# Kernel optimization log

Hardware: AMD Instinct MI355X
Metric: run time of the kernel (lower is better)

The kernel has to match this reference:

```python
import jax, jax.numpy as jnp
import numpy as np

# S=enc seq len (<= 2**ADD), B=batch, E=embed, H=hidden=controller, ADD=address bits,
# HA/HC = number of mode-1/mode-2 pointers, T=decode steps, OUT=out_size
S, B, E, H, ADD, HA, HC, T, OUT = 256, 128, 512, 512, 8, 2, 1, 64, 512
G = 3 * H  # GRU gate dim


def gru_cell(x, h, Wih, Whh, bih, bhh):
    gi = x @ Wih.T + bih
    gh = h @ Whh.T + bhh
    ir, iz, inn = jnp.split(gi, 3, -1)
    hr, hz, hn = jnp.split(gh, 3, -1)
    r = jax.nn.sigmoid(ir + hr)
    z = jax.nn.sigmoid(iz + hz)
    n = jnp.tanh(inn + r * hn)
    return (1.0 - z) * n + z * h


def run_gru(xs, h0, Wih, Whh, bih, bhh):
    def step(h, x):
        h2 = gru_cell(x, h, Wih, Whh, bih, bhh)
        return h2, h2
    return jax.lax.scan(step, h0, xs)


def setup_inputs():
    key = jax.random.key(0)
    ki = iter(jax.random.split(key, 48))
    def rn(shape, s=0.05):
        return jax.random.normal(next(ki), shape, jnp.float32) * s
    inp = {}
    inp['src'] = jax.random.normal(next(ki), (S, B, E), jnp.float32)
    inp['tgt'] = jax.random.normal(next(ki), (T, B, E), jnp.float32)
    # external address memory: 8-bit binary codes, rolled by a random start per batch
    rng = np.random.default_rng(0)
    base = ((np.arange(2 ** ADD)[:, None] & (1 << np.arange(ADD))[None, :]) != 0).astype(np.float32)
    starts = rng.integers(0, 2 ** ADD, size=B)
    A = np.stack([np.roll(base, int(s), axis=0)[:S] for s in starts], axis=1)  # (S,B,ADD)
    inp['A'] = jnp.asarray(A)
    # encoder bidirectional GRU
    inp['enc_Wih_f'] = rn((G, E)); inp['enc_Whh_f'] = rn((G, H))
    inp['enc_bih_f'] = rn((G,)); inp['enc_bhh_f'] = rn((G,))
    inp['enc_Wih_b'] = rn((G, E)); inp['enc_Whh_b'] = rn((G, H))
    inp['enc_bih_b'] = rn((G,)); inp['enc_bhh_b'] = rn((G,))
    # decoder Bahdanau attention
    inp['dec_attn_W'] = rn((H, 2 * H)); inp['dec_attn_b'] = rn((H,)); inp['dec_attn_v'] = rn((H,))
    # decoder GRU: input = [embedded(E + HA*H), context(H)]
    DIN = E + HA * H + H
    inp['dec_Wih'] = rn((G, DIN)); inp['dec_Whh'] = rn((G, H))
    inp['dec_bih'] = rn((G,)); inp['dec_bhh'] = rn((G,))
    inp['dec_out_W'] = rn((H, 2 * H)); inp['dec_out_b'] = rn((H,))
    # pointer units (stacked over HA)
    inp['pu_Wih'] = rn((HA, G, ADD)); inp['pu_Whh'] = rn((HA, G, H))
    inp['pu_bih'] = rn((HA, G)); inp['pu_bhh'] = rn((HA, G))
    inp['pu_qW'] = rn((HA, H, H)); inp['pu_qb'] = rn((HA, H))
    inp['pu_AmapW'] = rn((HA, ADD, ADD)); inp['pu_Amapb'] = rn((HA, ADD))
    inp['pu_qproj'] = rn((HA, H, H)); inp['pu_kproj'] = rn((HA, H, ADD)); inp['pu_vproj'] = rn((HA, H, H))
    inp['pu_inb'] = rn((HA, 3 * H))
    inp['pu_oproj'] = rn((HA, H, H)); inp['pu_ob'] = rn((HA, H))
    # content-based attention (add_att, 1 head)
    inp['aa_qproj'] = rn((H, H)); inp['aa_kproj'] = rn((H, H)); inp['aa_vproj'] = rn((H, H))
    inp['aa_inb'] = rn((3 * H,))
    inp['aa_oproj'] = rn((H, H)); inp['aa_ob'] = rn((H,))
    # tohs (HC=1) and output head
    inp['toh_W'] = rn((H, HA * H)); inp['toh_b'] = rn((H,))
    inp['out_W'] = rn((OUT, H * (HA + 1 + HC))); inp['out_b'] = rn((OUT,))
    inp['target_length'] = T
    return inp


def _forward(src, tgt, A,
             enc_Wih_f, enc_Whh_f, enc_bih_f, enc_bhh_f,
             enc_Wih_b, enc_Whh_b, enc_bih_b, enc_bhh_b,
             dec_attn_W, dec_attn_b, dec_attn_v,
             dec_Wih, dec_Whh, dec_bih, dec_bhh, dec_out_W, dec_out_b,
             pu_Wih, pu_Whh, pu_bih, pu_bhh, pu_qW, pu_qb, pu_AmapW, pu_Amapb,
             pu_qproj, pu_kproj, pu_vproj, pu_inb, pu_oproj, pu_ob,
             aa_qproj, aa_kproj, aa_vproj, aa_inb, aa_oproj, aa_ob,
             toh_W, toh_b, out_W, out_b):
    h0 = jnp.zeros((B, H), src.dtype)
    hTf, ysf = run_gru(src, h0, enc_Wih_f, enc_Whh_f, enc_bih_f, enc_bhh_f)
    hTb, ysb = run_gru(src[::-1], h0, enc_Wih_b, enc_Whh_b, enc_bih_b, enc_bhh_b)
    enc = ysf + ysb[::-1]                      # (S,B,H) sum of directions
    enc_bsh = jnp.swapaxes(enc, 0, 1)          # (B,S,H)
    A_bsa = A.reshape(B, S, ADD)               # faithful to torch .view(A.shape[1], A.shape[0], -1)
    scale = 1.0 / jnp.sqrt(jnp.asarray(H, src.dtype))
    # hoisted step-invariant K/V projections for the HA pointer units
    pu_bq, pu_bk, pu_bv = jnp.split(pu_inb, 3, axis=-1)                       # (HA,H) each
    Am = jnp.einsum('sba,uca->usbc', A, pu_AmapW) + pu_Amapb[:, None, None, :]
    Kp = jnp.einsum('usba,uha->usbh', Am, pu_kproj) + pu_bk[:, None, None, :]  # (HA,S,B,H)
    Vp = jnp.einsum('sbe,uhe->usbh', enc, pu_vproj) + pu_bv[:, None, None, :]  # (HA,S,B,H)
    aa_bq, aa_bk, aa_bv = jnp.split(aa_inb, 3)
    Kc = enc @ aa_kproj.T + aa_bk              # (S,B,H)
    Vc = enc @ aa_vproj.T + aa_bv

    def punit(ptr, hid, Wih, Whh, bih, bhh, qW, qb, qproj, bq, Kpu, Vpu, oproj, ob):
        hid2 = gru_cell(ptr, hid, Wih, Whh, bih, bhh)              # (B,H)
        q = (hid2 @ qW.T + qb) @ qproj.T + bq                       # (B,H)
        aw = jax.nn.softmax(jnp.einsum('bh,sbh->bs', q, Kpu) * scale, -1)
        cur_val = jnp.einsum('bs,sbh->bh', aw, Vpu) @ oproj.T + ob  # (B,H)
        cur_add = jnp.einsum('bs,bsa->ba', aw, A_bsa)               # (B,ADD)
        return cur_val, cur_add, hid2

    punit_v = jax.vmap(punit)

    ptrs0 = jnp.stack([A[0] if i % 2 == 0 else A[S - 1] for i in range(HA)])  # (HA,B,ADD)
    hida0 = jnp.zeros((HA, B, H), src.dtype)
    carry0 = (tgt[0], hTf, hida0, ptrs0)

    def step(carry, trg_t):
        out_emb, dec_h, hida, ptrs = carry
        cv1, cadd, hida2 = punit_v(ptrs, hida, pu_Wih, pu_Whh, pu_bih, pu_bhh,
                                   pu_qW, pu_qb, pu_qproj, pu_bq, Kp, Vp, pu_oproj, pu_ob)
        cv1_cat = jnp.swapaxes(cv1, 0, 1).reshape(B, HA * H)
        # Bahdanau attention of decoder hidden over encoder outputs
        cat = jnp.concatenate([jnp.broadcast_to(dec_h[:, None, :], (B, S, H)), enc_bsh], -1)
        energy = jax.nn.relu(cat @ dec_attn_W.T + dec_attn_b)       # (B,S,H)
        aw = jax.nn.softmax(energy @ dec_attn_v, -1)                # (B,S)
        ctx = jnp.einsum('bs,bsh->bh', aw, enc_bsh)
        rnn_in = jnp.concatenate([out_emb, cv1_cat, ctx], -1)       # [embedded, context]
        dec_h2 = gru_cell(rnn_in, dec_h, dec_Wih, dec_Whh, dec_bih, dec_bhh)
        dec_out = jnp.concatenate([dec_h2, ctx], -1) @ dec_out_W.T + dec_out_b  # (B,H)
        # content-based pointer (HC=1)
        qc = (cv1_cat @ toh_W.T + toh_b) @ aa_qproj.T + aa_bq
        awc = jax.nn.softmax(jnp.einsum('bh,sbh->bs', qc, Kc) * scale, -1)
        cv2 = jnp.einsum('bs,sbh->bh', awc, Vc) @ aa_oproj.T + aa_ob
        out_t = jnp.concatenate([dec_out, cv1_cat, cv2], -1) @ out_W.T + out_b
        return (trg_t, dec_h2, hida2, cadd), out_t

    _, outs = jax.lax.scan(step, carry0, tgt)
    return outs  # (T,B,OUT)


def reference(src, tgt, A,
              enc_Wih_f, enc_Whh_f, enc_bih_f, enc_bhh_f,
              enc_Wih_b, enc_Whh_b, enc_bih_b, enc_bhh_b,
              dec_attn_W, dec_attn_b, dec_attn_v,
              dec_Wih, dec_Whh, dec_bih, dec_bhh, dec_out_W, dec_out_b,
              pu_Wih, pu_Whh, pu_bih, pu_bhh, pu_qW, pu_qb, pu_AmapW, pu_Amapb,
              pu_qproj, pu_kproj, pu_vproj, pu_inb, pu_oproj, pu_ob,
              aa_qproj, aa_kproj, aa_vproj, aa_inb, aa_oproj, aa_ob,
              toh_W, toh_b, out_W, out_b, target_length):
    return _forward(src, tgt, A,
                    enc_Wih_f, enc_Whh_f, enc_bih_f, enc_bhh_f,
                    enc_Wih_b, enc_Whh_b, enc_bih_b, enc_bhh_b,
                    dec_attn_W, dec_attn_b, dec_attn_v,
                    dec_Wih, dec_Whh, dec_bih, dec_bhh, dec_out_W, dec_out_b,
                    pu_Wih, pu_Whh, pu_bih, pu_bhh, pu_qW, pu_qb, pu_AmapW, pu_Amapb,
                    pu_qproj, pu_kproj, pu_vproj, pu_inb, pu_oproj, pu_ob,
                    aa_qproj, aa_kproj, aa_vproj, aa_inb, aa_oproj, aa_ob,
                    toh_W, toh_b, out_W, out_b)
```

## Files before the change

kernel.cpp:

```cpp
#include <hip/hip_runtime.h>

typedef unsigned short u16;
typedef unsigned int u32;

#define DEVI __device__ __forceinline__

constexpr float SCALE_ATT = 0.04419417382415922f;

constexpr size_t OFF_GI    = 0;
constexpr size_t OFF_ENC   = OFF_GI    + 4ull*2*32*128*1536;
constexpr size_t OFF_EATT  = OFF_ENC   + 2ull*256*128*512;
constexpr size_t OFF_AM    = OFF_EATT  + 2ull*256*128*512;
constexpr size_t OFF_HF    = OFF_AM    + 4ull*2*256*128*8;
constexpr size_t OFF_HB    = OFF_HF    + 4ull*2*128*512;
constexpr size_t OFF_HFB   = OFF_HB    + 4ull*2*128*512;
constexpr size_t OFF_HBB   = OFF_HFB   + 2ull*2*128*512;
constexpr size_t OFF_HIDA  = OFF_HBB   + 2ull*2*128*512;
constexpr size_t OFF_HIDAB = OFF_HIDA  + 4ull*2*2*128*512;
constexpr size_t OFF_BAR   = OFF_HIDAB + 2ull*2*2*128*512;
constexpr size_t OFF_ZEND  = OFF_BAR   + 49152;
constexpr size_t OFF_DECH  = OFF_ZEND;
constexpr size_t OFF_DECHB = OFF_DECH  + 4ull*2*128*512;
constexpr size_t OFF_PTRS  = OFF_DECHB + 2ull*2*128*512;
constexpr size_t OFF_VPRE  = OFF_PTRS  + 4ull*2*128*8;
// ... 467 lines not shown
  const float* ap = Ain + ((size_t)b * 256 + t) * 8;
  float av[8];
  {
    float4 v0 = *(const float4*)ap;
    float4 v1 = *(const float4*)(ap + 4);
    av[0]=v0.x; av[1]=v0.y; av[2]=v0.z; av[3]=v0.w;
    av[4]=v1.x; av[5]=v1.y; av[6]=v1.z; av[7]=v1.w;
  }

  float inv[2];
  for (int u = 0; u < 2; u++){
    float s_ = su[u];
    float* sc = u ? sc1 : sc0;
    float m = s_;
    #pragma unroll
    for (int off = 32; off > 0; off >>= 1) m = fmaxf(m, __shfl_xor(m, off));
    if (lane == 0) red[w] = m;
    __syncthreads();
    float mx = fmaxf(fmaxf(red[0], red[1]), fmaxf(red[2], red[3]));
    float e = __expf(s_ - mx); sc[t] = e;
    float ca[9];
    ca[8] = e;
    #pragma unroll
    for (int a2 = 0; a2 < 8; a2++) ca[a2] = e * av[a2];
    #pragma unroll
    for (int j = 0; j < 9; j++){
      #pragma unroll
      for (int off = 32; off > 0; off >>= 1) ca[j] += __shfl_xor(ca[j], off);
    }
    if (lane == 0){
      #pragma unroll
      for (int j = 0; j < 9; j++) wred[w * 9 + j] = ca[j];
    }
    __syncthreads();
    if (t < 9){
      float v = wred[t] + wred[9 + t] + wred[18 + t] + wred[27 + t];
      if (t < 8) cd[u * 8 + t] = v;
      else red[4 + u] = v;
    }
    __syncthreads();
    inv[u] = 1.f / red[4 + u];
  }
  if (t < 8){
    st4_sys(&ptrs[((size_t)0 * 128 + b) * 8 + t], cd[t] * inv[0]);
    st4_sys(&ptrs[((size_t)128 + b) * 8 + t],     cd[8 + t] * inv[1]);
  }

  float a00 = 0.f, a01 = 0.f, a10 = 0.f, a11 = 0.f;
  const u16* ep = enc + (size_t)b * 512;
  #pragma unroll 16
  for (int s2 = 0; s2 < 256; s2++){
    float w0 = sc0[s2], w1 = sc1[s2];
    u32 pv = *(const u32*)(ep + (size_t)s2 * 65536 + 2 * t);
    float v0 = b2f((u16)pv);
    float v1 = b2f((u16)(pv >> 16));
    a00 += w0 * v0; a01 += w0 * v1; a10 += w1 * v0; a11 += w1 * v1;
  }
  float* vp = vpre + (size_t)b * 1024;
  st4_sys(&vp[2 * t], a00 * inv[0]);           st4_sys(&vp[2 * t + 1], a01 * inv[0]);
  st4_sys(&vp[512 + 2 * t], a10 * inv[1]);     st4_sys(&vp[512 + 2 * t + 1], a11 * inv[1]);
}

DEVI void dev_bahd(int b, const u16* eatt, const float* dpart, const float* vvec,
                   const u16* enc, float* ctx, float* fs)
{
  int t = threadIdx.x, lane = t & 63, w = t >> 6;
  float* dp = fs; float* vv = fs + 512; float* sc = fs + 1024; float* red = fs + 1280;
  dp[t] = ld4f_sys(dpart + (size_t)b * 512 + t);
  dp[t + 256] = ld4f_sys(dpart + (size_t)b * 512 + t + 256);
  vv[t] = vvec[t]; vv[t + 256] = vvec[t + 256];
  __syncthreads();
  float4 d0 = *(float4*)&dp[lane * 8], d1 = *(float4*)&dp[lane * 8 + 4];
  float4 v0 = *(float4*)&vv[lane * 8], v1 = *(float4*)&vv[lane * 8 + 4];
  for (int sb = 0; sb < 256; sb += 32){
    uint4 vl[8];
    #pragma unroll
    for (int i = 0; i < 8; i++){
      int s = sb + i * 4 + w;
      vl[i] = *(const uint4*)(eatt + ((size_t)s * 128 + b) * 512 + lane * 8);
    }
    #pragma unroll
    for (int i = 0; i < 8; i++){
      const u16* h = (const u16*)&vl[i];
      float r = fmaxf(0.f, b2f(h[0]) + d0.x) * v0.x + fmaxf(0.f, b2f(h[1]) + d0.y) * v0.y
              + fmaxf(0.f, b2f(h[2]) + d0.z) * v0.z + fmaxf(0.f, b2f(h[3]) + d0.w) * v0.w
              + fmaxf(0.f, b2f(h[4]) + d1.x) * v1.x + fmaxf(0.f, b2f(h[5]) + d1.y) * v1.y
              + fmaxf(0.f, b2f(h[6]) + d1.z) * v1.z + fmaxf(0.f, b2f(h[7]) + d1.w) * v1.w;
      #pragma unroll
      for (int off = 32; off > 0; off >>= 1) r += __shfl_xor(r, off);
      if (lane == 0) sc[sb + i * 4 + w] = r;
    }
  }
  __syncthreads();
  float s0 = sc[t];
  float m = s0;
  #pragma unroll
  for (int off = 32; off > 0; off >>= 1) m = fmaxf(m, __shfl_xor(m, off));
  if (lane == 0) red[w] = m;
  __syncthreads();
  float mx = fmaxf(fmaxf(red[0], red[1]), fmaxf(red[2], red[3]));
  float e = __expf(s0 - mx); sc[t] = e;
  float sum = e;
  #pragma unroll
  for (int off = 32; off > 0; off >>= 1) sum += __shfl_xor(sum, off);
  if (lane == 0) red[4 + w] = sum;
  __syncthreads();
  float inv = 1.f / (red[4] + red[5] + red[6] + red[7]);
  float a0 = 0.f, a1 = 0.f;
  const u16* ep = enc + (size_t)b * 512;
  #pragma unroll 16
  for (int s2 = 0; s2 < 256; s2++){
    float wgt = sc[s2];
    u32 pv = *(const u32*)(ep + (size_t)s2 * 65536 + 2 * t);
    a0 += wgt * b2f((u16)pv);
    a1 += wgt * b2f((u16)(pv >> 16));
  }
  st4_sys(&ctx[(size_t)b * 512 + 2 * t], a0 * inv);
  st4_sys(&ctx[(size_t)b * 512 + 2 * t + 1], a1 * inv);
}

DEVI void dev_cattn(int b, const float* qck, const u16* enc, float* cv2p, float* fs)
{
  int t = threadIdx.x, lane = t & 63, w = t >> 6;
  float* qv = fs; float* sc = fs + 1024; float* red = fs + 1280;
  qv[t] = ld4f_sys(qck + (size_t)b * 520 + t);
  qv[t + 256] = ld4f_sys(qck + (size_t)b * 520 + t + 256);
  __syncthreads();
  float qc0 = ld4f_sys(qck + (size_t)b * 520 + 512);
  float4 q0 = *(float4*)&qv[lane * 8], q1 = *(float4*)&qv[lane * 8 + 4];
  for (int sb = 0; sb < 256; sb += 32){
    uint4 vl[8];
    #pragma unroll
    for (int i = 0; i < 8; i++){
      int s = sb + i * 4 + w;
      vl[i] = *(const uint4*)(enc + ((size_t)s * 128 + b) * 512 + lane * 8);
    }
    #pragma unroll
    for (int i = 0; i < 8; i++){
      const u16* h = (const u16*)&vl[i];
      float r = b2f(h[0])*q0.x + b2f(h[1])*q0.y + b2f(h[2])*q0.z + b2f(h[3])*q0.w
              + b2f(h[4])*q1.x + b2f(h[5])*q1.y + b2f(h[6])*q1.z + b2f(h[7])*q1.w;
      #pragma unroll
      for (int off = 32; off > 0; off >>= 1) r += __shfl_xor(r, off);
      if (lane == 0) sc[sb + i * 4 + w] = (r + qc0) * SCALE_ATT;
    }
  }
  __syncthreads();
  float s0 = sc[t];
  float m = s0;
  #pragma unroll
  for (int off = 32; off > 0; off >>= 1) m = fmaxf(m, __shfl_xor(m, off));
  if (lane == 0) red[w] = m;
  __syncthreads();
  float mx = fmaxf(fmaxf(red[0], red[1]), fmaxf(red[2], red[3]));
  float e = __expf(s0 - mx); sc[t] = e;
  float sum = e;
  #pragma unroll
  for (int off = 32; off > 0; off >>= 1) sum += __shfl_xor(sum, off);
  if (lane == 0) red[4 + w] = sum;
  __syncthreads();
  float inv = 1.f / (red[4] + red[5] + red[6] + red[7]);
  float a0 = 0.f, a1 = 0.f;
  const u16* ep = enc + (size_t)b * 512;
  #pragma unroll 16
  for (int s2 = 0; s2 < 256; s2++){
    float wgt = sc[s2];
    u32 pv = *(const u32*)(ep + (size_t)s2 * 65536 + 2 * t);
    a0 += wgt * b2f((u16)pv);
    a1 += wgt * b2f((u16)(pv >> 16));
  }
  st4_sys(&cv2p[(size_t)b * 512 + 2 * t], a0 * inv);
  st4_sys(&cv2p[(size_t)b * 512 + 2 * t + 1], a1 * inv);
}

DEVI void dev_outcvt(int b, const float* outt, const float* outb2, float* dst)
{
  int t = threadIdx.x;
  #pragma unroll
  for (int rep = 0; rep < 2; rep++){
    int o = t + rep * 256;
    float s = ld4f_sys(outt + (size_t)b * 512 + o) + ld4f_sys(outt + 65536 + (size_t)b * 512 + o)
            + ld4f_sys(outt + 131072 + (size_t)b * 512 + o) + ld4f_sys(outt + 196608 + (size_t)b * 512 + o);
    dst[(size_t)b * 512 + o] = s + outb2[o];
  }
}

struct EncArgs {
  const float *WhhF, *WhhB, *giF, *giB;
  const float *bihF, *bhhF, *bihB, *bhhB;
  float *HF, *HB; u16 *HFB, *HBB, *ENC;
  u32 *BAR; int bar0;
  int s0;
};

__global__ __launch_bounds__(256) void k_enc(EncArgs a)
{
  __shared__ short Bw[24576];
  __shared__ short Al[4096];
  int blk = blockIdx.x;
  int d = blk >> 5, gt = blk & 31;
  int t = threadIdx.x, lane = t & 63, w = t >> 6;

  const float* Whh = d ? a.WhhB : a.WhhF;
  for (int c = t; c < 3072; c += 256){
    int brow = c >> 6, kc = c & 63;
    int grow = (brow >> 4) * 512 + gt * 16 + (brow & 15);
    const float* wp = Whh + (size_t)grow * 512 + kc * 8;
    *(uint4*)&Bw[((kc * 48) + brow) * 8] = cvt8(*(const float4*)wp, *(const float4*)(wp + 4));
  }
  const float* bih = d ? a.bihB : a.bihF;
  const float* bhh = d ? a.bhhB : a.bhhF;
  int gcol = gt * 16 + (lane & 15);
  float bir = bih[gcol],        bhr = bhh[gcol];
  float biz = bih[512 + gcol],  bhz = bhh[512 + gcol];
  float bin = bih[1024 + gcol], bhn = bhh[1024 + gcol];
  float* hf_base = d ? a.HB : a.HF;
  u16*   hb_base = d ? a.HBB : a.HFB;
  const float* gi_base = d ? a.giB : a.giF;
  __syncthreads();

  for (int si = 0; si < 32; si++){
    int s = a.s0 + si;
    const u16* hb = hb_base + (size_t)(s & 1) * 65536;
    const float* hf = hf_base + (size_t)(s & 1) * 65536;
    float* hnf = hf_base + (size_t)((s + 1) & 1) * 65536;
    u16* hnb = hb_base + (size_t)((s + 1) & 1) * 65536;
    u16* eacc = a.ENC + (size_t)(d ? 255 - s : s) * 65536;

    ffrag zz4 = {0.f, 0.f, 0.f, 0.f};
    ffrag acc[2][3];
    #pragma unroll
    for (int i = 0; i < 2; i++)
      #pragma unroll
      for (int j = 0; j < 3; j++) acc[i][j] = zz4;

    for (int ki = 0; ki < 16; ki++){
      int k0 = ki * 32;
      int row0 = t >> 2, kq0 = t & 3;
      int row1 = (t + 256) >> 2, kq1 = (t + 256) & 3;
      vu4 hv0, hv1;
      ld16_nw(hb + (size_t)row0 * 512 + k0 + kq0 * 8, hv0);
      ld16_nw(hb + (size_t)row1 * 512 + k0 + kq1 * 8, hv1);
      vm_drain();
      *(vu4*)&Al[(((row0 >> 4) << 6) + (kq0 << 4) + (row0 & 15)) * 8] = hv0;
      *(vu4*)&Al[(((row1 >> 4) << 6) + (kq1 << 4) + (row1 & 15)) * 8] = hv1;
      __syncthreads();
      bfrag af[2], bv[3];
      #pragma unroll
      for (int fr = 0; fr < 2; fr++) af[fr] = *(bfrag*)&Al[(((w * 2 + fr) * 64) + lane) * 8];
      #pragma unroll
      for (int fc = 0; fc < 3; fc++) bv[fc] = *(bfrag*)&Bw[(((ki * 4 + (lane >> 4)) * 48) + fc * 16 + (lane & 15)) * 8];
      #pragma unroll
      for (int fr = 0; fr < 2; fr++)
        #pragma unroll
        for (int fc = 0; fc < 3; fc++)
          acc[fr][fc] = __builtin_amdgcn_mfma_f32_16x16x32_bf16(af[fr], bv[fc], acc[fr][fc], 0, 0, 0);
      __syncthreads();
    }

    const float* gp0 = gi_base + (size_t)si * 196608;
    #pragma unroll
    for (int fr = 0; fr < 2; fr++){
      #pragma unroll
      for (int i = 0; i < 4; i++){
        int brow = w * 32 + fr * 16 + ((lane >> 4) << 2) + i;
        const float* gp = gp0 + (size_t)brow * 1536;
        float gr_ = gp[gcol], gz_ = gp[512 + gcol], gn_ = gp[1024 + gcol];
        float hold = ld4f_sys(hf + (size_t)brow * 512 + gcol);
        float r  = sigmf_(gr_ + acc[fr][0][i] + bir + bhr);
        float zg = sigmf_(gz_ + acc[fr][1][i] + biz + bhz);
        float n  = tanhf_(gn_ + bin + r * (acc[fr][2][i] + bhn));
        float hn = (1.f - zg) * n + zg * hold;
        size_t idx = (size_t)brow * 512 + gcol;
        st4_sys(hnf + idx, hn);
        st2_sys(hnb + idx, f2b(hn));
        eacc[idx] = f2b(b2f(eacc[idx]) + hn);
      }
    }
    gridbar2(a.BAR + BAR_ENCF, a.BAR + BAR_ENCGO, (u32)(a.s0 + si + 1), 64, blk, 0);
  }
}

struct DecArgs {
  const float *tgt, *Ag, *AM, *KA, *CAE, *dattW, *dattv;
  const float *puWhh, *puWih, *pubih, *pubhh;
  const float *dWhh, *DBIH2, *dbhh, *VKE2, *OUTB2;
  const u16 *ENC, *EATT, *DWF, *MKTW, *OWF;
  float *HIDA; u16 *HIDAB;
  float *DECH; u16 *DECHB;
  float *HF0; u16 *HFB0;
  float *PTRS, *VPRE, *CTX, *DPART, *QCK, *CV2P, *GIDEC, *OUTT, *out;
  u32 *BAR;
};

__global__ __launch_bounds__(256) void k_dec(DecArgs a)
{
  __shared__ short Al[4096];
  __shared__ short Bl[4096];
  __shared__ float fs[1600];
  const int blk = blockIdx.x;
  const Seg4 S4SENT = {nullptr, 0, 0, 1 << 30, 0};
  u32* dF = a.BAR + BAR_DECF;
  u32* dG = a.BAR + BAR_DECGO;
  const int GATHER = 200;

  for (int st = 0; st < 64; st++){
    const float* hida_c  = a.HIDA  + (size_t)(st & 1) * 131072;
    float*       hida_n  = a.HIDA  + (size_t)((st + 1) & 1) * 131072;
    const u16*   hidab_c = a.HIDAB + (size_t)(st & 1) * 131072;
    u16*         hidab_n = a.HIDAB + (size_t)((st + 1) & 1) * 131072;
    const float* dech_c  = (st == 0) ? a.HF0  : a.DECH  + (size_t)((st + 1) & 1) * 65536;
    const u16*   dechb_c = (st == 0) ? a.HFB0 : a.DECHB + (size_t)((st + 1) & 1) * 65536;
    float*       dech_n  = a.DECH  + (size_t)(st & 1) * 65536;
    u16*         dechb_n = a.DECHB + (size_t)(st & 1) * 65536;
    u32 seq0 = (u32)(st * 5);

    if (blk < 32){
      int u = blk >> 4, g0 = (blk & 15) * 32;
      dev_gru3<1>(g0, hidab_c + (size_t)u * 65536, hida_c + (size_t)u * 65536,
                  a.puWhh + (size_t)u * 786432, nullptr,
                  a.PTRS + u * 1024, a.puWih + (size_t)u * 12288,
                  a.pubih + u * 1536, a.pubhh + u * 1536,
                  hida_n + (size_t)u * 65536, hidab_n + (size_t)u * 65536, Al, Bl);
    } else if (blk < 40){
      Z4 z;
      z.sg[0] = {dechb_c, 512, 0, 512, 1}; z.sg[1] = S4SENT; z.sg[2] = S4SENT; z.sg[3] = S4SENT;
      z.Bp = a.dattW; z.ldb = 1024; z.bf32 = 1; z.bias = nullptr;
      z.Cp = a.DPART; z.ldc = 512; z.cslab = 0; z.N = 512; z.K = 512;
      dev_mfma4<64>(z, blk - 32, 0, 1, Al, Bl);
    } else if (blk < 168 && st > 0){
      dev_outcvt(blk - 40, a.OUTT, a.OUTB2, a.out + (size_t)(st - 1) * 65536);
    }
    gridbar2(dF, dG, seq0 + 1, 256, blk, GATHER);

    if (blk < 128){
      dev_puattn(blk, hida_n, a.KA, a.CAE, a.AM, a.Ag, a.ENC, a.VPRE, a.PTRS, fs);
    } else {
      dev_bahd(blk - 128, a.EATT, a.DPART, a.dattv, a.ENC, a.CTX, fs);
    }
    gridbar2(dF, dG, seq0 + 2, 256, blk, GATHER);

    if (blk < 48){
      Z4 z;
      z.sg[0] = {a.tgt + (size_t)(st ? st - 1 : 0) * 65536, 512, 1, 512, 0};
      z.sg[1] = {a.VPRE, 1024, 1, 1024, 1};
      z.sg[2] = {a.CTX, 512, 1, 512, 1};
      z.sg[3] = S4SENT;
      z.Bp = a.DWF; z.ldb = 2048; z.bf32 = 0; z.bias = nullptr;
      z.Cp = a.GIDEC; z.ldc = 1536; z.cslab = 196608; z.N = 1536; z.K = 2048;
      dev_mfma4<128>(z, blk % 12, blk / 12, 4, Al, Bl);
    } else if (blk < 57){
      Z4 z;
      z.sg[0] = {a.VPRE, 1024, 1, 1024, 1}; z.sg[1] = S4SENT; z.sg[2] = S4SENT; z.sg[3] = S4SENT;
      z.Bp = a.MKTW; z.ldb = 1024; z.bf32 = 0; z.bias = a.VKE2;
      z.Cp = a.QCK; z.ldc = 520; z.cslab = 0; z.N = 513; z.K = 1024;
      dev_mfma4<64>(z, blk - 48, 0, 1, Al, Bl);
    }
    gridbar2(dF, dG, seq0 + 3, 256, blk, GATHER);

    if (blk < 16){
      dev_gru3<2>(blk * 32, dechb_c, dech_c, a.dWhh, a.GIDEC, nullptr, nullptr,
                  a.DBIH2, a.dbhh, dech_n, dechb_n, Al, Bl);
    } else if (blk < 144){
      dev_cattn(blk - 16, a.QCK, a.ENC, a.CV2P, fs);
    }
    gridbar2(dF, dG, seq0 + 4, 256, blk, GATHER);

    if (blk < 32){
      Z4 z;
      z.sg[0] = {dechb_n, 512, 0, 512, 1};
      z.sg[1] = {a.CTX, 512, 1, 512, 1};
      z.sg[2] = {a.VPRE, 1024, 1, 1024, 1};
      z.sg[3] = {a.CV2P, 512, 1, 512, 1};
      z.Bp = a.OWF; z.ldb = 2560; z.bf32 = 0; z.bias = nullptr;
      z.Cp = a.OUTT; z.ldc = 512; z.cslab = 65536; z.N = 512; z.K = 2560;
      dev_mfma4<64>(z, blk & 7, blk >> 3, 4, Al, Bl);
    }
    gridbar2(dF, dG, seq0 + 5, 256, blk, GATHER);
  }
  if (blk < 128) dev_outcvt(blk, a.OUTT, a.OUTB2, a.out + 63ull * 65536);
}

struct Job {
  const float* A; const float* B; const float* D; void* C;
  int Asm, Ask, Bsk, Bsn, Dsm, Dsn, Csm, Csn;
  int cbf, M, N, K, kind;
};
struct Jobs { Job j[24]; int nj; long long off[25]; };

__global__ __launch_bounds__(256) void k_setup(Jobs J)
{
  long long total = J.off[J.nj];
  for (long long tid = (long long)blockIdx.x * 256 + threadIdx.x; tid < total; tid += (long long)gridDim.x * 256){
    int ji = 0;
    while (tid >= J.off[ji + 1]) ji++;
    Job jb = J.j[ji];
    long long l = tid - J.off[ji];
    if (jb.kind == 0){
      int m = (int)(l / jb.N), n = (int)(l - (long long)m * jb.N);
      float acc = 0.f;
      const float* ap = jb.A + (size_t)m * jb.Asm;
      const float* bp = jb.B + (size_t)n * jb.Bsn;
      for (int k = 0; k < jb.K; k++)
        acc += ap[(size_t)k * jb.Ask] * bp[(size_t)k * jb.Bsk];
      if (jb.D) acc += jb.D[(size_t)m * jb.Dsm + (size_t)n * jb.Dsn];
      if (jb.cbf) ((u16*)jb.C)[(size_t)m * jb.Csm + (size_t)n * jb.Csn] = f2b(acc);
      else ((float*)jb.C)[(size_t)m * jb.Csm + (size_t)n * jb.Csn] = acc;
    } else if (jb.kind == 1){
      int m = (int)(l / jb.N), n = (int)(l - (long long)m * jb.N);
      ((u16*)jb.C)[(size_t)m * jb.Csm + (size_t)n * jb.Csn] = f2b(jb.A[(size_t)m * jb.Asm + (size_t)n * jb.Ask]);
    } else if (jb.kind == 2){
      int u = (int)(l >> 15), sb = (int)(l & 32767);
      float x[8];
      #pragma unroll
      for (int a2 = 0; a2 < 8; a2++) x[a2] = jb.A[(size_t)sb * 8 + a2];
      float* op = (float*)jb.C + ((size_t)u * 32768 + sb) * 8;
      #pragma unroll
      for (int c = 0; c < 8; c++){
        float acc = jb.D[u * 8 + c];
        #pragma unroll
        for (int a2 = 0; a2 < 8; a2++) acc += x[a2] * jb.B[(u * 8 + c) * 8 + a2];
        op[c] = acc;
      }
    } else {
      int u = (int)(l >> 10), r = (int)(l & 1023);
      int bb = r >> 3, aa = r & 7;
      int su = u ? 255 : 0;
      ((float*)jb.C)[l] = jb.A[((size_t)su * 128 + bb) * 8 + aa];
    }
  }
}

static inline Seg mkseg(const void* p, int ld, int f32, int K){ Seg s; s.p = p; s.ld = ld; s.f32 = f32; s.K = K; return s; }
static const Seg SENT = {nullptr, 0, 0, 1 << 30};

static inline void addJ(Jobs& JS, Job jb, long long cnt){
  JS.j[JS.nj] = jb;
  JS.off[JS.nj + 1] = JS.off[JS.nj] + cnt;
  JS.nj++;
}
static inline Job JG(const float* A, int Asm, int Ask, const float* B, int Bsk, int Bsn,
                     const float* D, int Dsm, int Dsn, void* C, int Csm, int Csn,
                     int cbf, int M, int N, int K, int kind = 0){
  Job j; j.A=A; j.B=B; j.D=D; j.C=C; j.Asm=Asm; j.Ask=Ask; j.Bsk=Bsk; j.Bsn=Bsn;
  j.Dsm=Dsm; j.Dsn=Dsn; j.Csm=Csm; j.Csn=Csn; j.cbf=cbf; j.M=M; j.N=N; j.K=K; j.kind=kind;
  return j;
}

extern "C" void kernel_launch(void* const* d_in, const int* in_sizes, int n_in,
                              void* d_out, int out_size, void* d_ws, size_t ws_size,
                              hipStream_t stream)
{
  (void)in_sizes; (void)out_size;
  if (n_in < 44 || ws_size < WS_NEED) return;

  const float* src   = (const float*)d_in[0];
  const float* tgt   = (const float*)d_in[1];
  const float* Ag    = (const float*)d_in[2];
  const float* eWihF = (const float*)d_in[3];
  const float* eWhhF = (const float*)d_in[4];
  const float* ebihF = (const float*)d_in[5];
  const float* ebhhF = (const float*)d_in[6];
  const float* eWihB = (const float*)d_in[7];
  const float* eWhhB = (const float*)d_in[8];
  const float* ebihB = (const float*)d_in[9];
  const float* ebhhB = (const float*)d_in[10];
  const float* dattW = (const float*)d_in[11];
  const float* dattb = (const float*)d_in[12];
  const float* dattv = (const float*)d_in[13];
  const float* dWih  = (const float*)d_in[14];
  const float* dWhh  = (const float*)d_in[15];
  const float* dbih  = (const float*)d_in[16];
  const float* dbhh  = (const float*)d_in[17];
  const float* doW   = (const float*)d_in[18];
  const float* dob   = (const float*)d_in[19];
  const float* puWih = (const float*)d_in[20];
  const float* puWhh = (const float*)d_in[21];
  const float* pubih = (const float*)d_in[22];
  const float* pubhh = (const float*)d_in[23];
  const float* puqW  = (const float*)d_in[24];
  const float* puqb  = (const float*)d_in[25];
  const float* puAW  = (const float*)d_in[26];
  const float* puAb  = (const float*)d_in[27];
  const float* puqp  = (const float*)d_in[28];
  const float* pukp  = (const float*)d_in[29];
  const float* puvp  = (const float*)d_in[30];
  const float* puinb = (const float*)d_in[31];
  const float* puop  = (const float*)d_in[32];
  const float* puob  = (const float*)d_in[33];
  const float* aaq   = (const float*)d_in[34];
  const float* aak   = (const float*)d_in[35];
  const float* aav   = (const float*)d_in[36];
  const float* aainb = (const float*)d_in[37];
  const float* aao   = (const float*)d_in[38];
  const float* aaob  = (const float*)d_in[39];
  const float* tohW  = (const float*)d_in[40];
  const float* tohb  = (const float*)d_in[41];
  const float* outW  = (const float*)d_in[42];
  const float* outb  = (const float*)d_in[43];

  char* ws = (char*)d_ws;
  float* GI    = (float*)(ws + OFF_GI);
  u16*   ENC   = (u16*)(ws + OFF_ENC);
  u16*   EATT  = (u16*)(ws + OFF_EATT);
  float* AM    = (float*)(ws + OFF_AM);
  float* HF    = (float*)(ws + OFF_HF);
  float* HB    = (float*)(ws + OFF_HB);
  u16*   HFB   = (u16*)(ws + OFF_HFB);
  u16*   HBB   = (u16*)(ws + OFF_HBB);
  float* HIDA  = (float*)(ws + OFF_HIDA);
  u16*   HIDAB = (u16*)(ws + OFF_HIDAB);
  u32*   BAR   = (u32*)(ws + OFF_BAR);
  float* DECH  = (float*)(ws + OFF_DECH);
  u16*   DECHB = (u16*)(ws + OFF_DECHB);
  float* PTRS  = (float*)(ws + OFF_PTRS);
  float* VPRE  = (float*)(ws + OFF_VPRE);
  float* CTX   = (float*)(ws + OFF_CTX);
  float* DPART = (float*)(ws + OFF_DPART);
  float* QCK   = (float*)(ws + OFF_QCK);
  float* CV2P  = (float*)(ws + OFF_CV2P);
  float* GIDEC = (float*)(ws + OFF_GIDEC);
  float* OUTT  = (float*)(ws + OFF_OUTT);
  float* WOVF  = (float*)(ws + OFF_WOVF);
  float* WOVCF = (float*)(ws + OFF_WOVCF);
  float* MKTF  = (float*)(ws + OFF_MKTF);
  u16*   DWF   = (u16*)(ws + OFF_DWF);
  u16*   MKTW  = (u16*)(ws + OFF_MKTW);
  u16*   OWF   = (u16*)(ws + OFF_OWF);
  float* BOV   = (float*)(ws + OFF_BOV);
  float* BOVC  = (float*)(ws + OFF_BOVC);
  float* KAx   = (float*)(ws + OFF_KA);
  float* CAE   = (float*)(ws + OFF_CAE);
  float* RT    = (float*)(ws + OFF_RT);
  float* BQC   = (float*)(ws + OFF_BQC);
  float* PMAT  = (float*)(ws + OFF_PMAT);
  float* CQ    = (float*)(ws + OFF_CQ);
  float* VKE2  = (float*)(ws + OFF_VKE2);
  float* DBIH2 = (float*)(ws + OFF_DBIH2);
  float* OUTB2 = (float*)(ws + OFF_OUTB2);

  hipMemsetAsync(ENC, 0, 2ull*256*128*512, stream);
  hipMemsetAsync(ws + OFF_HF, 0, OFF_ZEND - OFF_HF, stream);

  {
    Jobs S{}; S.nj = 0; S.off[0] = 0;
    for (int u = 0; u < 2; u++){
      const float* qp  = puqp + (size_t)u * 262144;
      const float* kp  = pukp + (size_t)u * 4096;
      float* RTu = RT + u * 8192;
      addJ(S, JG(qp, 1, 512, kp, 8, 1, nullptr, 0, 0, RTu, 16, 1, 0, 512, 8, 512), 4096);
      addJ(S, JG(qp, 1, 512, puinb + u*1536 + 512, 1, 0, nullptr, 0, 0, RTu + 8, 16, 1, 0, 512, 1, 512), 512);
      addJ(S, JG(qp, 512, 1, puqb + u*512, 1, 0, puinb + u*1536, 1, 0, BQC + u*512, 1, 1, 0, 512, 1, 512), 512);
      addJ(S, JG(puop + (size_t)u*262144, 512, 1, puvp + (size_t)u*262144, 512, 1, nullptr, 0, 0, WOVF + (size_t)u*262144, 512, 1, 0, 512, 512, 512), 262144);
      addJ(S, JG(puop + (size_t)u*262144, 512, 1, puinb + u*1536 + 1024, 1, 0, puob + u*512, 1, 0, BOV + u*512, 1, 1, 0, 512, 1, 512), 512);
    }
    addJ(S, JG(aao, 512, 1, aav, 512, 1, nullptr, 0, 0, WOVCF, 512, 1, 0, 512, 512, 512), 262144);
    addJ(S, JG(aao, 512, 1, aainb + 1024, 1, 0, aaob, 1, 0, BOVC, 1, 1, 0, 512, 1, 512), 512);
    addJ(S, JG(aaq, 1, 512, aak, 512, 1, nullptr, 0, 0, PMAT, 516, 1, 0, 512, 512, 512), 262144);
    addJ(S, JG(aaq, 1, 512, aainb + 512, 1, 0, nullptr, 0, 0, PMAT + 512, 516, 1, 0, 512, 1, 512), 512);
    addJ(S, JG(aaq, 512, 1, tohb, 1, 0, aainb, 1, 0, CQ, 1, 1, 0, 512, 1, 512), 512);
    addJ(S, JG(dWih, 2048, 1, nullptr, 0, 0, nullptr, 0, 0, DWF, 2048, 1, 1, 1536, 512, 0, 1), 786432);
    addJ(S, JG(dWih + 1536, 2048, 1, nullptr, 0, 0, nullptr, 0, 0, DWF + 1536, 2048, 1, 1, 1536, 512, 0, 1), 786432);
    addJ(S, JG(outW, 2048, 1, doW, 1024, 1, nullptr, 0, 0, OWF, 2560, 1, 1, 512, 1024, 512), 524288);
    addJ(S, JG(outW, 2048, 1, dob, 1, 0, outb, 1, 0, OUTB2, 1, 1, 0, 512, 1, 512), 512);
    addJ(S, JG(Ag, 0, 0, puAW, 0, 0, puAb, 0, 0, AM, 0, 0, 0, 0, 0, 0, 2), 65536);
    addJ(S, JG(Ag, 0, 0, nullptr, 0, 0, nullptr, 0, 0, PTRS, 0, 0, 0, 0, 0, 0, 3), 2048);
    k_setup<<<2048, 256, 0, stream>>>(S);
  }
  {
    Jobs S{}; S.nj = 0; S.off[0] = 0;
    for (int u = 0; u < 2; u++){
      const float* kp = pukp + (size_t)u * 4096;
      addJ(S, JG(puqW + (size_t)u*262144, 1, 512, RT + u*8192, 16, 1, nullptr, 0, 0, KAx + u*8192, 16, 1, 0, 512, 9, 512), 4608);
      addJ(S, JG(BQC + u*512, 0, 1, kp, 8, 1, nullptr, 0, 0, CAE + u*16, 0, 1, 0, 1, 8, 512), 8);
      addJ(S, JG(BQC + u*512, 0, 1, puinb + u*1536 + 512, 1, 0, nullptr, 0, 0, CAE + u*16 + 8, 0, 1, 0, 1, 1, 512), 1);
      addJ(S, JG(dWih + 512 + u*512, 2048, 1, WOVF + (size_t)u*262144, 512, 1, nullptr, 0, 0, DWF + 512 + u*512, 2048, 1, 1, 1536, 512, 512), 786432);
      addJ(S, JG(outW + 512 + u*512, 2048, 1, WOVF + (size_t)u*262144, 512, 1, nullptr, 0, 0, OWF + 1024 + u*512, 2560, 1, 1, 512, 512, 512), 262144);
    }
    addJ(S, JG(tohW, 1, 1024, PMAT, 516, 1, nullptr, 0, 0, MKTF, 1, 1024, 0, 1024, 513, 512), 525312);
    addJ(S, JG(CQ, 0, 1, aak, 512, 1, nullptr, 0, 0, VKE2, 0, 1, 0, 1, 512, 512), 512);
    addJ(S, JG(CQ, 0, 1, aainb + 512, 1, 0, nullptr, 0, 0, VKE2 + 512, 0, 1, 0, 1, 1, 512), 1);
    addJ(S, JG(dWih + 512, 2048, 1, BOV, 1, 0, dbih, 1, 0, DBIH2, 1, 1, 0, 1536, 1, 1024), 1536);
    addJ(S, JG(outW + 1536, 2048, 1, WOVCF, 512, 1, nullptr, 0, 0, OWF + 2048, 2560, 1, 1, 512, 512, 512), 262144);
    addJ(S, JG(outW + 512, 2048, 1, BOV, 1, 0, OUTB2, 1, 0, OUTB2, 1, 1, 0, 512, 1, 1536), 512);
    k_setup<<<2048, 256, 0, stream>>>(S);
  }
  {
    Jobs S{}; S.nj = 0; S.off[0] = 0;
    for (int u = 0; u < 2; u++)
      addJ(S, JG(MKTF + u*512, 1024, 1, WOVF + (size_t)u*262144, 512, 1, nullptr, 0, 0, MKTW + u*512, 1024, 1, 1, 513, 512, 512), 262656);
    addJ(S, JG(MKTF, 1024, 1, BOV, 1, 0, VKE2, 1, 0, VKE2, 1, 1, 0, 513, 1, 1024), 513);
    k_setup<<<1024, 256, 0, stream>>>(S);
  }

  for (int c = 0; c < 8; c++){
    int c0 = c * 32;
    NTA nt{};
    nt.tilesN = 12;
    for (int d = 0; d < 2; d++){
      NTZ& zz = nt.z[d];
      zz.sg[0] = mkseg(d == 0 ? (const void*)(src + (size_t)c0 * 65536) : (const void*)src, 512, 1, 512);
      zz.sg[1] = SENT; zz.sg[2] = SENT;
      zz.Bp = d ? eWihB : eWihF; zz.ldb = 512; zz.bf32 = 1;
      zz.bias = nullptr; zz.biasf32 = 0;
      zz.Cp = GI + (size_t)d * 6291456; zz.ldc = 1536; zz.cf32 = 1; zz.cslab = 0;
      zz.N = 1536; zz.rev_s0 = (d == 0) ? -1 : (255 - c0); zz.K = 512;
    }
    k_mfma_nt<128><<<dim3(32*12, 1, 2), 256, 0, stream>>>(nt);

    EncArgs ea;
    ea.WhhF = eWhhF; ea.WhhB = eWhhB;
    ea.giF = GI; ea.giB = GI + 6291456;
    ea.bihF = ebihF; ea.bhhF = ebhhF; ea.bihB = ebihB; ea.bhhB = ebhhB;
    ea.HF = HF; ea.HB = HB; ea.HFB = HFB; ea.HBB = HBB; ea.ENC = ENC;
    ea.BAR = BAR; ea.bar0 = c * 32;
    ea.s0 = c0;
    k_enc<<<dim3(64), dim3(256), 0, stream>>>(ea);
  }

  {
    NTA nt{};
    nt.tilesN = 4;
    NTZ& zz = nt.z[0];
    zz.sg[0] = mkseg(ENC, 512, 0, 512); zz.sg[1] = SENT; zz.sg[2] = SENT;
    zz.Bp = dattW + 512; zz.ldb = 1024; zz.bf32 = 1;
    zz.bias = dattb; zz.biasf32 = 1;
    zz.Cp = EATT; zz.ldc = 512; zz.cf32 = 0; zz.cslab = 0;
    zz.N = 512; zz.rev_s0 = -1; zz.K = 512;
    k_mfma_nt<128><<<dim3(256*4, 1, 1), 256, 0, stream>>>(nt);
  }

  {
    DecArgs da;
    da.tgt = tgt; da.Ag = Ag; da.AM = AM; da.KA = KAx; da.CAE = CAE;
    da.dattW = dattW; da.dattv = dattv;
    da.puWhh = puWhh; da.puWih = puWih; da.pubih = pubih; da.pubhh = pubhh;
    da.dWhh = dWhh; da.DBIH2 = DBIH2; da.dbhh = dbhh; da.VKE2 = VKE2; da.OUTB2 = OUTB2;
    da.ENC = ENC; da.EATT = EATT; da.DWF = DWF; da.MKTW = MKTW; da.OWF = OWF;
    da.HIDA = HIDA; da.HIDAB = HIDAB; da.DECH = DECH; da.DECHB = DECHB;
    da.HF0 = HF; da.HFB0 = HFB;
    da.PTRS = PTRS; da.VPRE = VPRE; da.CTX = CTX; da.DPART = DPART;
    da.QCK = QCK; da.CV2P = CV2P; da.GIDEC = GIDEC; da.OUTT = OUTT;
    da.out = (float*)d_out;
    da.BAR = BAR;
    k_dec<<<dim3(256), dim3(256), 0, stream>>>(da);
  }
}
```

Before: 22.81 ms.

## Software-pipeline decoder step to remove one grid barrier per step

Moves the pointer-unit GRU for step st+1 and the decoder attention-projection GEMM for the next step into earlier phases of the current step, run on otherwise idle blocks. The prologue computes step 0's versions before the loop. This cuts the grid barriers per decode step from five to four, and the output conversion moves to another phase. It also raises the barrier GATHER parameter. The risk is data hazards: the PU GRU for st+1 now runs right after puattn reads hida_n, and those reads must be complete before the buffers are overwritten.

```diff
diff --git a/kernel.cpp b/kernel.cpp
--- a/kernel.cpp
+++ b/kernel.cpp
@@ -793,43 +793,49 @@
   const Seg4 S4SENT = {nullptr, 0, 0, 1 << 30, 0};
   u32* dF = a.BAR + BAR_DECF;
   u32* dG = a.BAR + BAR_DECGO;
-  const int GATHER = 200;
+  const int GATHER = 230;
+
+  #define PU_GRU(s_, u_, g0_) do { \
+    int s__ = (s_); int u__ = (u_); \
+    const u16*  pc_ = a.HIDAB + (size_t)(s__ & 1) * 131072 + (size_t)u__ * 65536; \
+    const float* pf_ = a.HIDA  + (size_t)(s__ & 1) * 131072 + (size_t)u__ * 65536; \
+    float* pn_  = a.HIDA  + (size_t)((s__ + 1) & 1) * 131072 + (size_t)u__ * 65536; \
+    u16*   pnb_ = a.HIDAB + (size_t)((s__ + 1) & 1) * 131072 + (size_t)u__ * 65536; \
+    dev_gru3<1>((g0_), pc_, pf_, a.puWhh + (size_t)u__ * 786432, nullptr, \
+                a.PTRS + u__ * 1024, a.puWih + (size_t)u__ * 12288, \
+                a.pubih + u__ * 1536, a.pubhh + u__ * 1536, pn_, pnb_, Al, Bl); \
+  } while(0)
+
+  #define DPART_GEMM(srcb_, tn_) do { \
+    Z4 z_; \
+    z_.sg[0] = {(srcb_), 512, 0, 512, 1}; z_.sg[1] = S4SENT; z_.sg[2] = S4SENT; z_.sg[3] = S4SENT; \
+    z_.Bp = a.dattW; z_.ldb = 1024; z_.bf32 = 1; z_.bias = nullptr; \
+    z_.Cp = a.DPART; z_.ldc = 512; z_.cslab = 0; z_.N = 512; z_.K = 512; \
+    dev_mfma4<64>(z_, (tn_), 0, 1, Al, Bl); \
+  } while(0)
+
+  if (blk < 32){
+    int u = blk >> 4, g0 = (blk & 15) * 32;
+    PU_GRU(0, u, g0);
+  } else if (blk < 40){
+    DPART_GEMM(a.HFB0, blk - 32);
+  }
+  gridbar2(dF, dG, 1u, 256, blk, GATHER);
 
   for (int st = 0; st < 64; st++){
-    const float* hida_c  = a.HIDA  + (size_t)(st & 1) * 131072;
-    float*       hida_n  = a.HIDA  + (size_t)((st + 1) & 1) * 131072;
-    const u16*   hidab_c = a.HIDAB + (size_t)(st & 1) * 131072;
-    u16*         hidab_n = a.HIDAB + (size_t)((st + 1) & 1) * 131072;
     const float* dech_c  = (st == 0) ? a.HF0  : a.DECH  + (size_t)((st + 1) & 1) * 65536;
     const u16*   dechb_c = (st == 0) ? a.HFB0 : a.DECHB + (size_t)((st + 1) & 1) * 65536;
     float*       dech_n  = a.DECH  + (size_t)(st & 1) * 65536;
     u16*         dechb_n = a.DECHB + (size_t)(st & 1) * 65536;
-    u32 seq0 = (u32)(st * 5);
-
-    if (blk < 32){
-      int u = blk >> 4, g0 = (blk & 15) * 32;
-      dev_gru3<1>(g0, hidab_c + (size_t)u * 65536, hida_c + (size_t)u * 65536,
-                  a.puWhh + (size_t)u * 786432, nullptr,
-                  a.PTRS + u * 1024, a.puWih + (size_t)u * 12288,
-                  a.pubih + u * 1536, a.pubhh + u * 1536,
-                  hida_n + (size_t)u * 65536, hidab_n + (size_t)u * 65536, Al, Bl);
-    } else if (blk < 40){
-      Z4 z;
-      z.sg[0] = {dechb_c, 512, 0, 512, 1}; z.sg[1] = S4SENT; z.sg[2] = S4SENT; z.sg[3] = S4SENT;
-      z.Bp = a.dattW; z.ldb = 1024; z.bf32 = 1; z.bias = nullptr;
-      z.Cp = a.DPART; z.ldc = 512; z.cslab = 0; z.N = 512; z.K = 512;
-      dev_mfma4<64>(z, blk - 32, 0, 1, Al, Bl);
-    } else if (blk < 168 && st > 0){
-      dev_outcvt(blk - 40, a.OUTT, a.OUTB2, a.out + (size_t)(st - 1) * 65536);
-    }
-    gridbar2(dF, dG, seq0 + 1, 256, blk, GATHER);
+    const float* hida_n  = a.HIDA  + (size_t)((st + 1) & 1) * 131072;
+    u32 seq0 = 2u + (u32)(st * 4);
 
     if (blk < 128){
       dev_puattn(blk, hida_n, a.KA, a.CAE, a.AM, a.Ag, a.ENC, a.VPRE, a.PTRS, fs);
     } else {
       dev_bahd(blk - 128, a.EATT, a.DPART, a.dattv, a.ENC, a.CTX, fs);
     }
-    gridbar2(dF, dG, seq0 + 2, 256, blk, GATHER);
+    gridbar2(dF, dG, seq0 + 0, 256, blk, GATHER);
 
     if (blk < 48){
       Z4 z;
@@ -846,8 +852,15 @@
       z.Bp = a.MKTW; z.ldb = 1024; z.bf32 = 0; z.bias = a.VKE2;
       z.Cp = a.QCK; z.ldc = 520; z.cslab = 0; z.N = 513; z.K = 1024;
       dev_mfma4<64>(z, blk - 48, 0, 1, Al, Bl);
-    }
-    gridbar2(dF, dG, seq0 + 3, 256, blk, GATHER);
+    } else if (blk < 89){
+      if (st < 63){
+        int u = (blk - 57) >> 4, g0 = ((blk - 57) & 15) * 32;
+        PU_GRU(st + 1, u, g0);
+      }
+    } else if (blk < 217 && st > 0){
+      dev_outcvt(blk - 89, a.OUTT, a.OUTB2, a.out + (size_t)(st - 1) * 65536);
+    }
+    gridbar2(dF, dG, seq0 + 1, 256, blk, GATHER);
 
     if (blk < 16){
       dev_gru3<2>(blk * 32, dechb_c, dech_c, a.dWhh, a.GIDEC, nullptr, nullptr,
@@ -855,7 +868,7 @@
     } else if (blk < 144){
       dev_cattn(blk - 16, a.QCK, a.ENC, a.CV2P, fs);
     }
-    gridbar2(dF, dG, seq0 + 4, 256, blk, GATHER);
+    gridbar2(dF, dG, seq0 + 2, 256, blk, GATHER);
 
     if (blk < 32){
       Z4 z;
@@ -866,10 +879,14 @@
       z.Bp = a.OWF; z.ldb = 2560; z.bf32 = 0; z.bias = nullptr;
       z.Cp = a.OUTT; z.ldc = 512; z.cslab = 65536; z.N = 512; z.K = 2560;
       dev_mfma4<64>(z, blk & 7, blk >> 3, 4, Al, Bl);
-    }
-    gridbar2(dF, dG, seq0 + 5, 256, blk, GATHER);
+    } else if (blk < 40){
+      if (st < 63) DPART_GEMM(dechb_n, blk - 32);
+    }
+    gridbar2(dF, dG, seq0 + 3, 256, blk, GATHER);
   }
   if (blk < 128) dev_outcvt(blk, a.OUTT, a.OUTB2, a.out + 63ull * 65536);
+  #undef PU_GRU
+  #undef DPART_GEMM
 }
 
 struct Job {
```

Result: faster. 20.73 ms (-9.1%).
